# Kernel optimization log

Hardware: AMD Instinct MI355X
Metric: run time of the kernel (lower is better)

Reference implementation:

```python
import jax, jax.numpy as jnp
import numpy as np

NUM_STAB = 1e-3  # numerical_stabilizer for relu kernel


def _relu_feature(x, proj):
    # x: [B, L, H, D], proj: [M, D] -> [B, L, H, M]
    ratio = 1.0 / jnp.sqrt(jnp.asarray(proj.shape[0], x.dtype))
    return jax.nn.relu(ratio * jnp.einsum('blhd,md->blhm', x, proj)) + NUM_STAB


def setup_inputs() -> dict:
    key = jax.random.key(0)
    k1, k2, k3, k4, k5 = jax.random.split(key, 5)
    B, L, H, D, M = 16, 576, 12, 64, 8  # L = length_of_side**2 = 24**2
    return {
        'query': jax.random.normal(k1, (B, L, H, D), dtype=jnp.float32),
        'key': jax.random.normal(k2, (B, L, H, D), dtype=jnp.float32),
        'value': jax.random.normal(k3, (B, L, H, D), dtype=jnp.float32),
        'projection_matrix': jax.random.normal(k4, (M, D), dtype=jnp.float32),
        # RPE mask is nonnegative per-head mixing matrix [H, L, L]
        'mask_matrix': jax.random.uniform(k5, (H, L, L), dtype=jnp.float32),
    }


def reference(query, key, value, projection_matrix, mask_matrix):
    # ReLU kernel features (projection_matrix_type='relu')
    q_prime = _relu_feature(query, projection_matrix)  # [B, L, H, M]
    k_prime = _relu_feature(key, projection_matrix)    # [B, L, H, M]
    B, L, H, M = k_prime.shape
    D = value.shape[-1]

    # D_1[b,l,h,m,d] = k'[b,l,h,m] * v[b,l,h,d], flattened over (m,d)
    D_1 = jnp.einsum('blhm,blhd->blhmd', k_prime, value).reshape(B, L, H, M * D)
    # mask-matrix causal/RPE mixing over the L dimension (per head)
    D_1_hat = jnp.einsum('hij,bjhc->bihc', mask_matrix, D_1).reshape(B, L, H, M, D)
    D_2_hat = jnp.einsum('hij,bjhm->bihm', mask_matrix, k_prime)  # [B, L, H, M]

    av_attention = jnp.einsum('blhm,blhmd->blhd', q_prime, D_1_hat)  # [B, L, H, D]
    ks_sum = jnp.sum(D_2_hat, axis=1)                                # [B, H, M]
    normalizer = jnp.einsum('blhm,bhm->blh', q_prime, ks_sum)        # [B, L, H]
    return av_attention / normalizer[..., None]
```

## Files before the change

kernel.cpp:

```cpp
#include <hip/hip_runtime.h>
#include <hip/hip_bf16.h>


#define B_ 16
#define L_ 576
#define H_ 12
#define D_ 64
#define M_ 8
#define NUM_STAB 1e-3f
#define RATIO 0.35355339059327373f

typedef __attribute__((ext_vector_type(8))) short short8;
typedef __attribute__((ext_vector_type(4))) float f32x4;

union Pack {
    uint4 u4;
    short8 s8;
    uint2 u2[2];
    unsigned u[4];
    unsigned short us[8];
};

__device__ inline unsigned short f2bf(float x) {
    union { float f; unsigned u; } a; a.f = x;
    unsigned r = (a.u + 0x7FFFu + ((a.u >> 16) & 1u)) >> 16;
    return (unsigned short)r;
}
__device__ inline unsigned pk2(float lo, float hi) {
    __hip_bfloat162 h = __float22bfloat162_rn(make_float2(lo, hi));
    union { __hip_bfloat162 b; unsigned u; } c; c.b = h;
    return c.u;
}
__device__ inline float bf2f(unsigned short u) {
    union { unsigned u; float f; } c; c.u = (unsigned)u << 16; return c.f;
}

#define WS_W_OFF  (H_ * L_)
#define WS_QP_OFF (H_ * L_ + B_ * H_ * M_)
#define QP_ELEMS  ((size_t)B_ * H_ * L_ * M_)

__global__ __launch_bounds__(256) void feat_kernel(const float* __restrict__ q,
                                                   const float* __restrict__ k,
                                                   const float* __restrict__ proj,
                                                   const float* __restrict__ mask,
                                                   unsigned short* __restrict__ qp,
                                                   unsigned short* __restrict__ kp,
                                                   float* __restrict__ cmask) {
    __shared__ float cred[4][16];
    const int lc = blockIdx.x, h = blockIdx.y, b = blockIdx.z, t = threadIdx.x;
    const int wv = t >> 6, l = t & 63, r8 = l >> 3, c8 = l & 7;
    const int row = lc * 32 + wv * 8 + r8;

    float4 pj0[8], pj1[8];
#pragma unroll
    for (int m = 0; m < 8; ++m) {
        pj0[m] = *(const float4*)(proj + m * 64 + c8 * 8);
        pj1[m] = *(const float4*)(proj + m * 64 + c8 * 8 + 4);
    }

#pragma unroll
    for (int s = 0; s < 2; ++s) {
        const float* src = s ? k : q;
        unsigned short* dst = s ? kp : qp;
        const float* xp = src + (((size_t)b * L_ + row) * H_ + h) * D_ + c8 * 8;
        float4 x0 = *(const float4*)xp;
        float4 x1 = *(const float4*)(xp + 4);
        x0.x *= RATIO; x0.y *= RATIO; x0.z *= RATIO; x0.w *= RATIO;
        x1.x *= RATIO; x1.y *= RATIO; x1.z *= RATIO; x1.w *= RATIO;
        float p[8];
#pragma unroll
        for (int m = 0; m < 8; ++m) {
            p[m] = x0.x * pj0[m].x + x0.y * pj0[m].y + x0.z * pj0[m].z + x0.w * pj0[m].w
                 + x1.x * pj1[m].x + x1.y * pj1[m].y + x1.z * pj1[m].z + x1.w * pj1[m].w;
        }
#pragma unroll
        for (int st = 1; st <= 4; st <<= 1) {
#pragma unroll
            for (int m = 0; m < 8; ++m) p[m] += __shfl_xor(p[m], st, 64);
        }
        float r = p[0];
        r = (c8 == 1) ? p[1] : r;
        r = (c8 == 2) ? p[2] : r;
        r = (c8 == 3) ? p[3] : r;
        r = (c8 == 4) ? p[4] : r;
        r = (c8 == 5) ? p[5] : r;
        r = (c8 == 6) ? p[6] : r;
        r = (c8 == 7) ? p[7] : r;
        r = fmaxf(r, 0.f) + NUM_STAB;
        dst[((size_t)(b * H_ + h) * L_ + row) * 8 + c8] = f2bf(r);
    }

    if (b < 2) {
        const int c = t & 15, rg = t >> 4;
        const int col0 = lc * 32 + b * 16;
        const float* mb = mask + (size_t)h * L_ * L_ + col0 + c;
        float a = 0.f;
#pragma unroll 4
        for (int k2 = 0; k2 < 36; ++k2) a += mb[(size_t)(rg + 16 * k2) * L_];
        a += __shfl_xor(a, 16, 64);
        a += __shfl_xor(a, 32, 64);
        if ((l >> 4) == 0) cred[wv][c] = a;
        __syncthreads();
        if (t < 16) cmask[h * L_ + col0 + t] = cred[0][t] + cred[1][t] + cred[2][t] + cred[3][t];
    }
}

__global__ __launch_bounds__(64) void wsum_kernel(const unsigned short* __restrict__ kp,
                                                  const float* __restrict__ cmask,
                                                  float* __restrict__ wbuf) {
    const int bh = blockIdx.x, lx = threadIdx.x;
    const int h = bh % H_;
    const unsigned short* kpb = kp + (size_t)bh * L_ * 8;
    const float* cm = cmask + h * L_;
    float a[8] = {0.f, 0.f, 0.f, 0.f, 0.f, 0.f, 0.f, 0.f};
    for (int j = lx; j < L_; j += 64) {
        const float c = cm[j];
        Pack pk; pk.u4 = *(const uint4*)(kpb + (size_t)j * 8);
#pragma unroll
        for (int m = 0; m < 8; ++m) a[m] += c * bf2f(pk.us[m]);
    }
#pragma unroll
    for (int st = 1; st < 64; st <<= 1) {
#pragma unroll
        for (int m = 0; m < 8; ++m) a[m] += __shfl_xor(a[m], st, 64);
    }
    float r = a[0];
    r = (lx == 1) ? a[1] : r;
    r = (lx == 2) ? a[2] : r;
    r = (lx == 3) ? a[3] : r;
    r = (lx == 4) ? a[4] : r;
    r = (lx == 5) ? a[5] : r;
    r = (lx == 6) ? a[6] : r;
    r = (lx == 7) ? a[7] : r;
    if (lx < 8) wbuf[(size_t)bh * 8 + lx] = r;
}

__global__ __launch_bounds__(256, 4) void attn_kernel(const float* __restrict__ v,
                                                      const float* __restrict__ mask,
                                                      const unsigned short* __restrict__ qp,
                                                      const unsigned short* __restrict__ kp,
                                                      const float* __restrict__ wbuf,
                                                      float* __restrict__ out) {
    __shared__ __align__(16) unsigned short Sp[4 * 16 * 64];
    __shared__ __align__(16) unsigned short Bt[2][64 * 64];

    const int t = threadIdx.x;
    int id = blockIdx.x;
    const int bhi = id & 7; id >>= 3;
    const int blo = id & 1; id >>= 1;
    const int it = id % 9, h = id / 9;
    const int b = bhi * 2 + blo;
    const int i0 = it * 64;

    const int wv = t >> 6, l = t & 63, c15 = l & 15, kq = l >> 4;

    const float* maskbase = mask + (size_t)h * L_ * L_ + (size_t)(i0 + 16 * wv + c15) * L_ + 4 * kq;
    const unsigned short* kpb = kp + (size_t)(b * H_ + h) * L_ * 8;
    const float* vb = v + ((size_t)b * L_ * H_ + h) * D_ + l;

    char* SpB = (char*)Sp + wv * 2048;
    const int sxor = (c15 & 7) << 4;
    const int lxor = (l & 7) << 4;

    short8 Bq;
    {
        Pack pk; pk.u4 = make_uint4(0, 0, 0, 0);
        if (kq == 0)
            pk.u4 = *(const uint4*)(qp + ((size_t)(b * H_ + h) * L_ + i0 + 16 * wv + c15) * 8);
        Bq = pk.s8;
    }

    f32x4 acc0 = {0.f, 0.f, 0.f, 0.f}, acc1 = acc0, acc2 = acc0, acc3 = acc0;
    const f32x4 zz = {0.f, 0.f, 0.f, 0.f};

    float vf[16];
    float4 mv0, mv1, mv2, mv3;
    uint4 a0 = make_uint4(0, 0, 0, 0), a1 = a0, a2 = a0, a3 = a0;
    {
#pragma unroll
        for (int qv = 0; qv < 16; ++qv) vf[qv] = vb[(size_t)(16 * wv + qv) * (H_ * D_)];
        mv0 = *(const float4*)(maskbase + 0);
        mv1 = *(const float4*)(maskbase + 16);
        mv2 = *(const float4*)(maskbase + 32);
        mv3 = *(const float4*)(maskbase + 48);
        if (kq == 0) {
            a0 = *(const uint4*)(kpb + (size_t)(c15) * 8);
            a1 = *(const uint4*)(kpb + (size_t)(16 + c15) * 8);
            a2 = *(const uint4*)(kpb + (size_t)(32 + c15) * 8);
            a3 = *(const uint4*)(kpb + (size_t)(48 + c15) * 8);
        }
    }

    for (int jt = 0; jt < 9; ++jt) {
        const int slab = jt & 1;
        char* BtB = (char*)Bt[slab];

        f32x4 s0, s1, s2, s3;
        {
            Pack p0, p1, p2, p3;
            p0.u4 = a0; p1.u4 = a1; p2.u4 = a2; p3.u4 = a3;
            __builtin_amdgcn_s_setprio(1);
            s0 = __builtin_amdgcn_mfma_f32_16x16x32_bf16(p0.s8, Bq, zz, 0, 0, 0);
            s1 = __builtin_amdgcn_mfma_f32_16x16x32_bf16(p1.s8, Bq, zz, 0, 0, 0);
            s2 = __builtin_amdgcn_mfma_f32_16x16x32_bf16(p2.s8, Bq, zz, 0, 0, 0);
            s3 = __builtin_amdgcn_mfma_f32_16x16x32_bf16(p3.s8, Bq, zz, 0, 0, 0);
            __builtin_amdgcn_s_setprio(0);
        }

        {
            Pack p0, p1;
#pragma unroll
            for (int qv = 0; qv < 4; ++qv) p0.u[qv] = pk2(vf[2 * qv], vf[2 * qv + 1]);
#pragma unroll
            for (int qv = 0; qv < 4; ++qv) p1.u[qv] = pk2(vf[8 + 2 * qv], vf[9 + 2 * qv]);
            const int base = l * 128 + 32 * wv;
            *(uint4*)(BtB + ((base) ^ lxor)) = p0.u4;
            *(uint4*)(BtB + ((base + 16) ^ lxor)) = p1.u4;
        }

        {
            const int sb = c15 * 128 + 8 * kq;
            uint2 st2;
            st2.x = pk2(s0[0] * mv0.x, s0[1] * mv0.y);
            st2.y = pk2(s0[2] * mv0.z, s0[3] * mv0.w);
            *(uint2*)(SpB + ((sb + 0) ^ sxor)) = st2;
            st2.x = pk2(s1[0] * mv1.x, s1[1] * mv1.y);
            st2.y = pk2(s1[2] * mv1.z, s1[3] * mv1.w);
            *(uint2*)(SpB + ((sb + 32) ^ sxor)) = st2;
            st2.x = pk2(s2[0] * mv2.x, s2[1] * mv2.y);
            st2.y = pk2(s2[2] * mv2.z, s2[3] * mv2.w);
            *(uint2*)(SpB + ((sb + 64) ^ sxor)) = st2;
            st2.x = pk2(s3[0] * mv3.x, s3[1] * mv3.y);
            st2.y = pk2(s3[2] * mv3.z, s3[3] * mv3.w);
            *(uint2*)(SpB + ((sb + 96) ^ sxor)) = st2;
        }

        __syncthreads();

        {
            const int j0n = ((jt < 8) ? jt + 1 : 0) * 64;
#pragma unroll
            for (int qv = 0; qv < 16; ++qv) vf[qv] = vb[(size_t)(j0n + 16 * wv + qv) * (H_ * D_)];
            mv0 = *(const float4*)(maskbase + j0n + 0);
            mv1 = *(const float4*)(maskbase + j0n + 16);
            mv2 = *(const float4*)(maskbase + j0n + 32);
            mv3 = *(const float4*)(maskbase + j0n + 48);
            if (kq == 0) {
                a0 = *(const uint4*)(kpb + (size_t)(j0n + c15) * 8);
                a1 = *(const uint4*)(kpb + (size_t)(j0n + 16 + c15) * 8);
                a2 = *(const uint4*)(kpb + (size_t)(j0n + 32 + c15) * 8);
                a3 = *(const uint4*)(kpb + (size_t)(j0n + 48 + c15) * 8);
            }
        }

        {
            short8 As0 = *(const short8*)(SpB + ((c15 * 128 + 16 * kq) ^ sxor));
            short8 As1 = *(const short8*)(SpB + ((c15 * 128 + 64 + 16 * kq) ^ sxor));
            __builtin_amdgcn_s_setprio(1);
#pragma unroll
            for (int di = 0; di < 4; ++di) {
                const int rb = (16 * di + c15) * 128;
                short8 B0 = *(const short8*)(BtB + ((rb + 16 * kq) ^ sxor));
                short8 B1 = *(const short8*)(BtB + ((rb + 64 + 16 * kq) ^ sxor));
                f32x4* ap = (di == 0) ? &acc0 : (di == 1) ? &acc1 : (di == 2) ? &acc2 : &acc3;
                *ap = __builtin_amdgcn_mfma_f32_16x16x32_bf16(As0, B0, *ap, 0, 0, 0);
                *ap = __builtin_amdgcn_mfma_f32_16x16x32_bf16(As1, B1, *ap, 0, 0, 0);
            }
            __builtin_amdgcn_s_setprio(0);
        }
    }

    const float* wp = wbuf + (size_t)(b * H_ + h) * 8;
    const float4 w0 = *(const float4*)wp;
    const float4 w1 = *(const float4*)(wp + 4);
    Pack pq;
    pq.u4 = *(const uint4*)(qp + ((size_t)(b * H_ + h) * L_ + i0 + 16 * wv + c15) * 8);
    float n = bf2f(pq.us[0]) * w0.x + bf2f(pq.us[1]) * w0.y +
              bf2f(pq.us[2]) * w0.z + bf2f(pq.us[3]) * w0.w +
              bf2f(pq.us[4]) * w1.x + bf2f(pq.us[5]) * w1.y +
              bf2f(pq.us[6]) * w1.z + bf2f(pq.us[7]) * w1.w;
    float iv[4];
#pragma unroll
    for (int r = 0; r < 4; ++r) iv[r] = 1.0f / __shfl(n, 4 * kq + r, 64);

    float* ob = out + (((size_t)b * L_ + i0 + 16 * wv + 4 * kq) * H_ + h) * D_ + c15;
    const f32x4 aa[4] = {acc0, acc1, acc2, acc3};
#pragma unroll
    for (int di = 0; di < 4; ++di)
#pragma unroll
        for (int r = 0; r < 4; ++r)
            ob[(size_t)r * (H_ * D_) + 16 * di] = aa[di][r] * iv[r];
}

extern "C" void kernel_launch(void* const* d_in, const int* in_sizes, int n_in,
                              void* d_out, int out_size, void* d_ws, size_t ws_size,
                              hipStream_t stream) {
    const float* q    = (const float*)d_in[0];
    const float* k    = (const float*)d_in[1];
    const float* v    = (const float*)d_in[2];
    const float* proj = (const float*)d_in[3];
    const float* mask = (const float*)d_in[4];
    float* out = (float*)d_out;

    float* ws = (float*)d_ws;
    float* cmask = ws;
    float* wbuf  = ws + WS_W_OFF;
    unsigned short* qp_w = (unsigned short*)(ws + WS_QP_OFF);
    unsigned short* kp_w = qp_w + QP_ELEMS;

    feat_kernel<<<dim3(L_ / 32, H_, B_), 256, 0, stream>>>(q, k, proj, mask, qp_w, kp_w, cmask);
    wsum_kernel<<<B_ * H_, 64, 0, stream>>>(kp_w, cmask, wbuf);
    attn_kernel<<<1728, 256, 0, stream>>>(v, mask, qp_w, kp_w, wbuf, out);
}
```

Baseline: 189.4 us.

## Split second GEMM by output columns so V operand stays in registers

```diff
diff --git a/kernel.cpp b/kernel.cpp
--- a/kernel.cpp
+++ b/kernel.cpp
@@ -141,8 +141,7 @@
                                                       const unsigned short* __restrict__ kp,
                                                       const float* __restrict__ wbuf,
                                                       float* __restrict__ out) {
-    __shared__ __align__(16) unsigned short Sp[4 * 16 * 64];
-    __shared__ __align__(16) unsigned short Bt[2][64 * 64];
+    __shared__ __align__(16) unsigned short Sp[2][4][16 * 64];
 
     const int t = threadIdx.x;
     int id = blockIdx.x;
@@ -153,14 +152,11 @@
     const int i0 = it * 64;
 
     const int wv = t >> 6, l = t & 63, c15 = l & 15, kq = l >> 4;
+    const int sxor = (c15 & 7) << 4;
 
     const float* maskbase = mask + (size_t)h * L_ * L_ + (size_t)(i0 + 16 * wv + c15) * L_ + 4 * kq;
     const unsigned short* kpb = kp + (size_t)(b * H_ + h) * L_ * 8;
-    const float* vb = v + ((size_t)b * L_ * H_ + h) * D_ + l;
-
-    char* SpB = (char*)Sp + wv * 2048;
-    const int sxor = (c15 & 7) << 4;
-    const int lxor = (l & 7) << 4;
+    const float* vbase = v + ((size_t)b * L_ * H_ + h) * D_ + 16 * wv + c15;
 
     short8 Bq;
     {
@@ -173,49 +169,37 @@
     f32x4 acc0 = {0.f, 0.f, 0.f, 0.f}, acc1 = acc0, acc2 = acc0, acc3 = acc0;
     const f32x4 zz = {0.f, 0.f, 0.f, 0.f};
 
-    float vf[16];
+    uint4 a0 = make_uint4(0, 0, 0, 0), a1 = a0, a2 = a0, a3 = a0;
     float4 mv0, mv1, mv2, mv3;
-    uint4 a0 = make_uint4(0, 0, 0, 0), a1 = a0, a2 = a0, a3 = a0;
-    {
-#pragma unroll
-        for (int qv = 0; qv < 16; ++qv) vf[qv] = vb[(size_t)(16 * wv + qv) * (H_ * D_)];
-        mv0 = *(const float4*)(maskbase + 0);
-        mv1 = *(const float4*)(maskbase + 16);
-        mv2 = *(const float4*)(maskbase + 32);
-        mv3 = *(const float4*)(maskbase + 48);
-        if (kq == 0) {
-            a0 = *(const uint4*)(kpb + (size_t)(c15) * 8);
-            a1 = *(const uint4*)(kpb + (size_t)(16 + c15) * 8);
-            a2 = *(const uint4*)(kpb + (size_t)(32 + c15) * 8);
-            a3 = *(const uint4*)(kpb + (size_t)(48 + c15) * 8);
-        }
-    }
+    float vf0[8], vf1[8];
+
+    if (kq == 0) {
+        a0 = *(const uint4*)(kpb + (size_t)(c15) * 8);
+        a1 = *(const uint4*)(kpb + (size_t)(16 + c15) * 8);
+        a2 = *(const uint4*)(kpb + (size_t)(32 + c15) * 8);
+        a3 = *(const uint4*)(kpb + (size_t)(48 + c15) * 8);
+    }
+    mv0 = *(const float4*)(maskbase + 0);
+    mv1 = *(const float4*)(maskbase + 16);
+    mv2 = *(const float4*)(maskbase + 32);
+    mv3 = *(const float4*)(maskbase + 48);
+#pragma unroll
+    for (int e = 0; e < 8; ++e) vf0[e] = vbase[(size_t)(kq * 8 + e) * (H_ * D_)];
+#pragma unroll
+    for (int e = 0; e < 8; ++e) vf1[e] = vbase[(size_t)(32 + kq * 8 + e) * (H_ * D_)];
 
     for (int jt = 0; jt < 9; ++jt) {
         const int slab = jt & 1;
-        char* BtB = (char*)Bt[slab];
+        char* SpW = (char*)Sp[slab][wv];
 
         f32x4 s0, s1, s2, s3;
         {
             Pack p0, p1, p2, p3;
             p0.u4 = a0; p1.u4 = a1; p2.u4 = a2; p3.u4 = a3;
-            __builtin_amdgcn_s_setprio(1);
             s0 = __builtin_amdgcn_mfma_f32_16x16x32_bf16(p0.s8, Bq, zz, 0, 0, 0);
             s1 = __builtin_amdgcn_mfma_f32_16x16x32_bf16(p1.s8, Bq, zz, 0, 0, 0);
             s2 = __builtin_amdgcn_mfma_f32_16x16x32_bf16(p2.s8, Bq, zz, 0, 0, 0);
             s3 = __builtin_amdgcn_mfma_f32_16x16x32_bf16(p3.s8, Bq, zz, 0, 0, 0);
-            __builtin_amdgcn_s_setprio(0);
-        }
-
-        {
-            Pack p0, p1;
-#pragma unroll
-            for (int qv = 0; qv < 4; ++qv) p0.u[qv] = pk2(vf[2 * qv], vf[2 * qv + 1]);
-#pragma unroll
-            for (int qv = 0; qv < 4; ++qv) p1.u[qv] = pk2(vf[8 + 2 * qv], vf[9 + 2 * qv]);
-            const int base = l * 128 + 32 * wv;
-            *(uint4*)(BtB + ((base) ^ lxor)) = p0.u4;
-            *(uint4*)(BtB + ((base + 16) ^ lxor)) = p1.u4;
         }
 
         {
@@ -223,73 +207,78 @@
             uint2 st2;
             st2.x = pk2(s0[0] * mv0.x, s0[1] * mv0.y);
             st2.y = pk2(s0[2] * mv0.z, s0[3] * mv0.w);
-            *(uint2*)(SpB + ((sb + 0) ^ sxor)) = st2;
+            *(uint2*)(SpW + ((sb + 0) ^ sxor)) = st2;
             st2.x = pk2(s1[0] * mv1.x, s1[1] * mv1.y);
             st2.y = pk2(s1[2] * mv1.z, s1[3] * mv1.w);
-            *(uint2*)(SpB + ((sb + 32) ^ sxor)) = st2;
+            *(uint2*)(SpW + ((sb + 32) ^ sxor)) = st2;
             st2.x = pk2(s2[0] * mv2.x, s2[1] * mv2.y);
             st2.y = pk2(s2[2] * mv2.z, s2[3] * mv2.w);
-            *(uint2*)(SpB + ((sb + 64) ^ sxor)) = st2;
+            *(uint2*)(SpW + ((sb + 64) ^ sxor)) = st2;
             st2.x = pk2(s3[0] * mv3.x, s3[1] * mv3.y);
             st2.y = pk2(s3[2] * mv3.z, s3[3] * mv3.w);
-            *(uint2*)(SpB + ((sb + 96) ^ sxor)) = st2;
-        }
-
-        __syncthreads();
+            *(uint2*)(SpW + ((sb + 96) ^ sxor)) = st2;
+        }
+
+        Pack bv0, bv1;
+#pragma unroll
+        for (int q4 = 0; q4 < 4; ++q4) bv0.u[q4] = pk2(vf0[2 * q4], vf0[2 * q4 + 1]);
+#pragma unroll
+        for (int q4 = 0; q4 < 4; ++q4) bv1.u[q4] = pk2(vf1[2 * q4], vf1[2 * q4 + 1]);
+
+        asm volatile("s_waitcnt lgkmcnt(0)\n\ts_barrier" ::: "memory");
 
         {
             const int j0n = ((jt < 8) ? jt + 1 : 0) * 64;
-#pragma unroll
-            for (int qv = 0; qv < 16; ++qv) vf[qv] = vb[(size_t)(j0n + 16 * wv + qv) * (H_ * D_)];
-            mv0 = *(const float4*)(maskbase + j0n + 0);
-            mv1 = *(const float4*)(maskbase + j0n + 16);
-            mv2 = *(const float4*)(maskbase + j0n + 32);
-            mv3 = *(const float4*)(maskbase + j0n + 48);
             if (kq == 0) {
                 a0 = *(const uint4*)(kpb + (size_t)(j0n + c15) * 8);
                 a1 = *(const uint4*)(kpb + (size_t)(j0n + 16 + c15) * 8);
                 a2 = *(const uint4*)(kpb + (size_t)(j0n + 32 + c15) * 8);
                 a3 = *(const uint4*)(kpb + (size_t)(j0n + 48 + c15) * 8);
             }
+            mv0 = *(const float4*)(maskbase + j0n + 0);
+            mv1 = *(const float4*)(maskbase + j0n + 16);
+            mv2 = *(const float4*)(maskbase + j0n + 32);
+            mv3 = *(const float4*)(maskbase + j0n + 48);
+#pragma unroll
+            for (int e = 0; e < 8; ++e) vf0[e] = vbase[(size_t)(j0n + kq * 8 + e) * (H_ * D_)];
+#pragma unroll
+            for (int e = 0; e < 8; ++e) vf1[e] = vbase[(size_t)(j0n + 32 + kq * 8 + e) * (H_ * D_)];
         }
 
         {
-            short8 As0 = *(const short8*)(SpB + ((c15 * 128 + 16 * kq) ^ sxor));
-            short8 As1 = *(const short8*)(SpB + ((c15 * 128 + 64 + 16 * kq) ^ sxor));
-            __builtin_amdgcn_s_setprio(1);
-#pragma unroll
-            for (int di = 0; di < 4; ++di) {
-                const int rb = (16 * di + c15) * 128;
-                short8 B0 = *(const short8*)(BtB + ((rb + 16 * kq) ^ sxor));
-                short8 B1 = *(const short8*)(BtB + ((rb + 64 + 16 * kq) ^ sxor));
-                f32x4* ap = (di == 0) ? &acc0 : (di == 1) ? &acc1 : (di == 2) ? &acc2 : &acc3;
-                *ap = __builtin_amdgcn_mfma_f32_16x16x32_bf16(As0, B0, *ap, 0, 0, 0);
-                *ap = __builtin_amdgcn_mfma_f32_16x16x32_bf16(As1, B1, *ap, 0, 0, 0);
+            const char* SpR = (const char*)Sp[slab][0];
+            const int rb = c15 * 128;
+#pragma unroll
+            for (int iw = 0; iw < 4; ++iw) {
+                const char* ch = SpR + iw * 2048;
+                short8 As0 = *(const short8*)(ch + ((rb + 16 * kq) ^ sxor));
+                short8 As1 = *(const short8*)(ch + ((rb + 64 + 16 * kq) ^ sxor));
+                f32x4* ap = (iw == 0) ? &acc0 : (iw == 1) ? &acc1 : (iw == 2) ? &acc2 : &acc3;
+                *ap = __builtin_amdgcn_mfma_f32_16x16x32_bf16(As0, bv0.s8, *ap, 0, 0, 0);
+                *ap = __builtin_amdgcn_mfma_f32_16x16x32_bf16(As1, bv1.s8, *ap, 0, 0, 0);
             }
-            __builtin_amdgcn_s_setprio(0);
         }
     }
 
     const float* wp = wbuf + (size_t)(b * H_ + h) * 8;
     const float4 w0 = *(const float4*)wp;
     const float4 w1 = *(const float4*)(wp + 4);
-    Pack pq;
-    pq.u4 = *(const uint4*)(qp + ((size_t)(b * H_ + h) * L_ + i0 + 16 * wv + c15) * 8);
-    float n = bf2f(pq.us[0]) * w0.x + bf2f(pq.us[1]) * w0.y +
-              bf2f(pq.us[2]) * w0.z + bf2f(pq.us[3]) * w0.w +
-              bf2f(pq.us[4]) * w1.x + bf2f(pq.us[5]) * w1.y +
-              bf2f(pq.us[6]) * w1.z + bf2f(pq.us[7]) * w1.w;
-    float iv[4];
-#pragma unroll
-    for (int r = 0; r < 4; ++r) iv[r] = 1.0f / __shfl(n, 4 * kq + r, 64);
-
-    float* ob = out + (((size_t)b * L_ + i0 + 16 * wv + 4 * kq) * H_ + h) * D_ + c15;
     const f32x4 aa[4] = {acc0, acc1, acc2, acc3};
 #pragma unroll
-    for (int di = 0; di < 4; ++di)
-#pragma unroll
-        for (int r = 0; r < 4; ++r)
-            ob[(size_t)r * (H_ * D_) + 16 * di] = aa[di][r] * iv[r];
+    for (int iw = 0; iw < 4; ++iw) {
+        Pack pq;
+        pq.u4 = *(const uint4*)(qp + ((size_t)(b * H_ + h) * L_ + i0 + 16 * iw + c15) * 8);
+        float n = bf2f(pq.us[0]) * w0.x + bf2f(pq.us[1]) * w0.y +
+                  bf2f(pq.us[2]) * w0.z + bf2f(pq.us[3]) * w0.w +
+                  bf2f(pq.us[4]) * w1.x + bf2f(pq.us[5]) * w1.y +
+                  bf2f(pq.us[6]) * w1.z + bf2f(pq.us[7]) * w1.w;
+        float* ob = out + (((size_t)b * L_ + i0 + 16 * iw) * H_ + h) * D_ + 16 * wv + c15;
+#pragma unroll
+        for (int r = 0; r < 4; ++r) {
+            float iv = 1.0f / __shfl(n, 4 * kq + r, 64);
+            ob[(size_t)(4 * kq + r) * (H_ * D_)] = aa[iw][r] * iv;
+        }
+    }
 }
 
 extern "C" void kernel_launch(void* const* d_in, const int* in_sizes, int n_in,
```

New measurement: 188.1 us. About the same (-0.7%).
